# Optimization experiments

Measured on AMD Instinct MI355X. Metric: run time of the kernel, lower is better.

## Reference

```python
import jax, jax.numpy as jnp
import numpy as np

B, N = 4, 8192
EPS = 1e-5

def _gather(points, idx):
    # points: (B, N, C); idx: (B, ...) int -> (B, ..., C)
    return jax.vmap(lambda p, i: p[i])(points, idx)

def _square_distance(src, dst):
    # src: (B,S,3), dst: (B,N,3) -> (B,S,N)
    return (jnp.sum(src * src, -1)[..., None]
            + jnp.sum(dst * dst, -1)[:, None, :]
            - 2.0 * jnp.einsum('bsc,bnc->bsn', src, dst))

def _fps(xyz, npoint):
    # farthest point sampling, deterministic start at index 0
    b, n, _ = xyz.shape
    def step(carry, _):
        distance, farthest = carry
        centroid = _gather(xyz, farthest)                # (B,3)
        d = jnp.sum((xyz - centroid[:, None, :]) ** 2, -1)
        distance = jnp.minimum(distance, d)
        return (distance, jnp.argmax(distance, -1).astype(jnp.int32)), farthest
    init = (jnp.full((b, n), 1e10, xyz.dtype), jnp.zeros((b,), jnp.int32))
    _, idx = jax.lax.scan(step, init, None, length=npoint)
    return jnp.transpose(idx)                            # (B, npoint)

def _query_ball(radius, nsample, xyz, new_xyz):
    n = xyz.shape[1]
    sqrdists = _square_distance(new_xyz, xyz)            # (B,S,N)
    gi = jnp.where(sqrdists > radius * radius, n, jnp.arange(n, dtype=jnp.int32))
    gi = jnp.sort(gi, axis=-1)[:, :, :nsample]           # (B,S,K)
    first = gi[:, :, :1]
    return jnp.where(gi == n, first, gi)

def _set_abstraction(xyz, points, npoint, radius, nsample, w, bconv, gamma, beta):
    fps_idx = _fps(xyz, npoint)
    new_xyz = _gather(xyz, fps_idx)                      # (B,S,3)
    idx = _query_ball(radius, nsample, xyz, new_xyz)     # (B,S,K)
    grouped = _gather(xyz, idx) - new_xyz[:, :, None, :] # (B,S,K,3) centered
    if points is not None:
        grouped = jnp.concatenate([grouped, _gather(points, idx)], -1)
    # shared MLP = 1x1 Conv2d + BatchNorm2d (training batch stats) + ReLU
    h = jnp.einsum('bskc,cd->bskd', grouped, w) + bconv
    mu = jnp.mean(h, axis=(0, 1, 2))
    var = jnp.var(h, axis=(0, 1, 2))
    h = jax.nn.relu((h - mu) * jax.lax.rsqrt(var + EPS) * gamma + beta)
    return new_xyz, jnp.max(h, axis=2)                   # max-pool over nsample

def setup_inputs():
    key = jax.random.key(0)
    ks = jax.random.split(key, 5)
    return {
        'xyz': jax.random.uniform(ks[0], (B, N, 6), jnp.float32),
        'w1': jax.random.normal(ks[1], (6, 128), jnp.float32) * 0.1,
        'b1': jax.random.normal(ks[2], (128,), jnp.float32) * 0.01,
        'g1': jnp.ones((128,), jnp.float32),
        'be1': jnp.zeros((128,), jnp.float32),
        'w2': jax.random.normal(ks[3], (131, 693), jnp.float32) * 0.05,
        'b2': jax.random.normal(ks[4], (693,), jnp.float32) * 0.01,
        'g2': jnp.ones((693,), jnp.float32),
        'be2': jnp.zeros((693,), jnp.float32),
    }

def reference(xyz, w1, b1, g1, be1, w2, b2, g2, be2):
    coords, norm = xyz[:, :, :3], xyz[:, :, 3:]
    l1_xyz, l1_pts = _set_abstraction(coords, norm, 2048, 0.0025, 32, w1, b1, g1, be1)
    l2_xyz, l2_pts = _set_abstraction(l1_xyz, l1_pts, 256, 0.005, 16, w2, b2, g2, be2)
    return l2_xyz, l2_pts  # (B,256,3), (B,256,693)
```

## Files before the change

### kernel.cpp

```cpp
#include <hip/hip_runtime.h>
#include <hip/hip_bf16.h>

#define DEV __device__ __forceinline__

DEV float wave_max_f32(float v) {
#define STEPDPP(ctrl) { int iv = __float_as_int(v); \
    int sh = __builtin_amdgcn_update_dpp(iv, iv, ctrl, 0xf, 0xf, false); \
    v = fmaxf(v, __int_as_float(sh)); }
  STEPDPP(0x111)
  STEPDPP(0x112)
  STEPDPP(0x114)
  STEPDPP(0x118)
  STEPDPP(0x142)
  STEPDPP(0x143)
#undef STEPDPP
  return __int_as_float(__builtin_amdgcn_readlane(__float_as_int(v), 63));
}

__global__ void sentinel_k(float* out) {
  out[0] = 1000.0f;
}

__global__ __launch_bounds__(256) void zero_k(double* __restrict__ p, int n) {
  int i = blockIdx.x * 256 + threadIdx.x;
  if (i < n) p[i] = 0.0;
}

template<int PPT, int NPT, int NPTS, int STRIDE>
__global__ __launch_bounds__(512) void fps_k(const float* __restrict__ pts,
                                             float* __restrict__ out_xyz,
                                             float* __restrict__ out_f) {
  const int b = blockIdx.x, t = threadIdx.x;
  __shared__ unsigned long long wkey[2][8];
  __shared__ float wcx[2][8], wcy[2][8], wcz[2][8];
  float px[PPT], py[PPT], pz[PPT], dist[PPT];
  const int base = t * PPT;
  for (int j = 0; j < PPT; ++j) {
    const float* P = pts + (size_t)(b * NPTS + base + j) * STRIDE;
    px[j] = P[0]; py[j] = P[1]; pz[j] = P[2]; dist[j] = 1e10f;
  }
  if (t == 0) {
    wcx[1][0] = px[0]; wcy[1][0] = py[0]; wcz[1][0] = pz[0];
    size_t o = (size_t)b * NPT * 3;
    out_xyz[o] = px[0]; out_xyz[o+1] = py[0]; out_xyz[o+2] = pz[0];
    if (out_f) { out_f[o] = px[0]; out_f[o+1] = py[0]; out_f[o+2] = pz[0]; }
  }
  __syncthreads();
  float cx = wcx[1][0], cy = wcy[1][0], cz = wcz[1][0];
  const int lane = t & 63, wv = t >> 6;
  for (int s = 0; s < NPT - 1; ++s) {
    float vA = -1.0f, vB = -1.0f;
    int jA = 0, jB = PPT / 2;
    float axA = 0.f, ayA = 0.f, azA = 0.f, axB = 0.f, ayB = 0.f, azB = 0.f;
    {
#pragma clang fp contract(off)
      for (int j = 0; j < PPT / 2; ++j) {
        float dx = px[j] - cx, dy = py[j] - cy, dz = pz[j] - cz;
        float d = (dx*dx + dy*dy) + dz*dz;
        float dj = fminf(dist[j], d);
        dist[j] = dj;
        if (dj > vA) { vA = dj; jA = j; axA = px[j]; ayA = py[j]; azA = pz[j]; }
      }
      for (int j = PPT / 2; j < PPT; ++j) {
        float dx = px[j] - cx, dy = py[j] - cy, dz = pz[j] - cz;
        float d = (dx*dx + dy*dy) + dz*dz;
        float dj = fminf(dist[j], d);
        dist[j] = dj;
        if (dj > vB) { vB = dj; jB = j; axB = px[j]; ayB = py[j]; azB = pz[j]; }
      }
    }
    float vmax; int jb; float bx, by, bz;
    if (vB > vA) { vmax = vB; jb = jB; bx = axB; by = ayB; bz = azB; }
    else         { vmax = vA; jb = jA; bx = axA; by = ayA; bz = azA; }

    float wmax = wave_max_f32(vmax);
    unsigned long long mb = __ballot(vmax == wmax);
    int wl = __ffsll((unsigned long long)mb) - 1;
    const int p = s & 1;
    if (lane == wl) {
      wkey[p][wv] = ((unsigned long long)__float_as_uint(wmax) << 32) |
                    (unsigned long long)(0xFFFFFFFFu - (unsigned)(base + jb));
      wcx[p][wv] = bx; wcy[p][wv] = by; wcz[p][wv] = bz;
    }
    __syncthreads();
    unsigned long long bestk = wkey[p][0];
    int bw = 0;
#pragma unroll
    for (int w = 1; w < 8; ++w) {
      unsigned long long k2 = wkey[p][w];
      if (k2 > bestk) { bestk = k2; bw = w; }
    }
    cx = wcx[p][bw]; cy = wcy[p][bw]; cz = wcz[p][bw];
    if (t == 0) {
      size_t o = ((size_t)b * NPT + s + 1) * 3;
      out_xyz[o] = cx; out_xyz[o+1] = cy; out_xyz[o+2] = cz;
      if (out_f) { out_f[o] = cx; out_f[o+1] = cy; out_f[o+2] = cz; }
    }
  }
}

template<bool APPLY>
__global__ __launch_bounds__(256) void ball1_k(
    const float* __restrict__ xyz, const float* __restrict__ l1xyz,
    const float* __restrict__ w1, const float* __restrict__ b1,
    const double* __restrict__ A1, const double* __restrict__ B1,
    float* __restrict__ l1pts,
    double* __restrict__ S1R, double* __restrict__ S2R) {
  const int blk = blockIdx.x;
  const int b = blk >> 11, s = blk & 2047;
  const int t = threadIdx.x;
  __shared__ double w1s[768];
  __shared__ double b1s[128];
  __shared__ unsigned long long wm[4];
  __shared__ int lst[32];
  __shared__ double fls[32][6];
  __shared__ double red0[128], red1[128];

  for (int i = t; i < 768; i += 256) w1s[i] = (double)w1[i];
  if (t < 128) b1s[t] = (double)b1[t];

  const float* xb = xyz + (size_t)b * 8192 * 6;
  size_t co = ((size_t)b * 2048 + s) * 3;
  double cx = (double)l1xyz[co], cy = (double)l1xyz[co+1], cz = (double)l1xyz[co+2];

  const double R2 = 0.0025 * 0.0025;
  int cnt = 0;
  const int wvv = t >> 6, lane = t & 63;
  {
#pragma clang fp contract(off)
    double cs2 = (cx*cx + cy*cy) + cz*cz;
    for (int chunk = 0; chunk < 32 && cnt < 32; ++chunk) {
      int g = chunk * 256 + t;
      double x = (double)xb[(size_t)g*6];
      double y = (double)xb[(size_t)g*6+1];
      double z = (double)xb[(size_t)g*6+2];
      double pn2 = (x*x + y*y) + z*z;
      double dot = (cx*x + cy*y) + cz*z;
      double dsq = (cs2 + pn2) - 2.0 * dot;
      bool pred = !(dsq > R2);
      unsigned long long m = __ballot(pred);
      if (lane == 0) wm[wvv] = m;
      __syncthreads();
      int pre = 0, tot = 0;
      for (int w = 0; w < 4; ++w) {
        int c = __popcll(wm[w]);
        if (w < wvv) pre += c;
        tot += c;
      }
      if (pred) {
        int rank = cnt + pre + __popcll(m & ((1ull << lane) - 1ull));
        if (rank < 32) lst[rank] = g;
      }
      cnt += tot;
      __syncthreads();
    }
  }
  int cc = cnt < 32 ? cnt : 32;
  if (t >= cc && t < 32) lst[t] = lst[0];
  __syncthreads();
  if (t < 32) {
    int j = lst[t];
    fls[t][0] = (double)xb[(size_t)j*6]   - cx;
    fls[t][1] = (double)xb[(size_t)j*6+1] - cy;
    fls[t][2] = (double)xb[(size_t)j*6+2] - cz;
    fls[t][3] = (double)xb[(size_t)j*6+3];
    fls[t][4] = (double)xb[(size_t)j*6+4];
    fls[t][5] = (double)xb[(size_t)j*6+5];
  }
  __syncthreads();
  const int d = t & 127, kh = t >> 7;
  if (APPLY) {
    double a = A1[d], bb = B1[d];
    double vmax = -1e300;
    for (int k = kh; k < 32; k += 2) {
      double h = b1s[d];
#pragma unroll
      for (int c = 0; c < 6; ++c) h = fma(fls[k][c], w1s[c*128 + d], h);
      vmax = fmax(vmax, fma(a, h, bb));
    }
    if (kh == 1) red0[d] = vmax;
    __syncthreads();
    if (kh == 0) {
      double v = fmax(vmax, red0[d]);
      l1pts[((size_t)b * 2048 + s) * 128 + d] = (float)fmax(v, 0.0);
    }
  } else {
    double p1 = 0.0, p2 = 0.0;
    for (int k = kh; k < 32; k += 2) {
      double h = b1s[d];
#pragma unroll
      for (int c = 0; c < 6; ++c) h = fma(fls[k][c], w1s[c*128 + d], h);
      p1 += h; p2 = fma(h, h, p2);
    }
    if (kh == 1) { red0[d] = p1; red1[d] = p2; }
    __syncthreads();
    if (kh == 0) {
      int rep = blk & 7;
      atomicAdd(&S1R[(size_t)rep * 128 + d], p1 + red0[d]);
      atomicAdd(&S2R[(size_t)rep * 128 + d], p2 + red1[d]);
    }
  }
}

__global__ __launch_bounds__(256) void bn_finalize(const double* __restrict__ S1,
                                                   const double* __restrict__ S2,
                                                   int nrep, int D, double invN,
                                                   const float* __restrict__ g,
                                                   const float* __restrict__ be,
                                                   double* __restrict__ A, double* __restrict__ Bc) {
  int d = blockIdx.x * 256 + threadIdx.x;
  if (d >= D) return;
  double s1 = 0.0, s2 = 0.0;
  for (int r = 0; r < nrep; ++r) {
    s1 += S1[(size_t)r * D + d];
    s2 += S2[(size_t)r * D + d];
  }
  double mu = s1 * invN;
  double var = s2 * invN - mu * mu;
  double a = (double)g[d] / sqrt(var + 1e-5);
  A[d]  = a;
  Bc[d] = (double)be[d] - mu * a;
}

template<bool APPLY>
__global__ __launch_bounds__(256) void ball2_k(
    const float* __restrict__ l1xyz, const float* __restrict__ l1pts,
    const float* __restrict__ l2xyz,
    const float* __restrict__ w2, const float* __restrict__ b2,
    const double* __restrict__ A2, const double* __restrict__ B2,
    float* __restrict__ outp,
    double* __restrict__ T1R, double* __restrict__ T2R) {
  const int blk = blockIdx.x;
  const int b = blk >> 8, s = blk & 255;
  const int t = threadIdx.x;
  __shared__ double fT[131][16];
  __shared__ unsigned long long wm[4];
  __shared__ int lst[16];
  const float* Pb = l1xyz + (size_t)b * 2048 * 3;
  size_t co = ((size_t)b * 256 + s) * 3;
  double cx = (double)l2xyz[co], cy = (double)l2xyz[co+1], cz = (double)l2xyz[co+2];
  const double R2 = 0.005 * 0.005;
  int cnt = 0;
  const int wvv = t >> 6, lane = t & 63;
  {
#pragma clang fp contract(off)
    double cs2 = (cx*cx + cy*cy) + cz*cz;
    for (int chunk = 0; chunk < 8 && cnt < 16; ++chunk) {
      int g = chunk * 256 + t;
      double x = (double)Pb[(size_t)g*3];
      double y = (double)Pb[(size_t)g*3+1];
      double z = (double)Pb[(size_t)g*3+2];
      double pn2 = (x*x + y*y) + z*z;
      double dot = (cx*x + cy*y) + cz*z;
      double dsq = (cs2 + pn2) - 2.0 * dot;
      bool pred = !(dsq > R2);
      unsigned long long m = __ballot(pred);
      if (lane == 0) wm[wvv] = m;
      __syncthreads();
      int pre = 0, tot = 0;
      for (int w = 0; w < 4; ++w) {
        int c = __popcll(wm[w]);
        if (w < wvv) pre += c;
        tot += c;
      }
      if (pred) {
        int rank = cnt + pre + __popcll(m & ((1ull << lane) - 1ull));
        if (rank < 16) lst[rank] = g;
      }
      cnt += tot;
      __syncthreads();
    }
  }
  int cc = cnt < 16 ? cnt : 16;
  if (t >= cc && t < 16) lst[t] = lst[0];
  __syncthreads();
  for (int i = t; i < 16 * 131; i += 256) {
    int k = i & 15, c = i >> 4;
    int j = lst[k];
    double v;
    if (c == 0)      v = (double)Pb[(size_t)j*3]   - cx;
    else if (c == 1) v = (double)Pb[(size_t)j*3+1] - cy;
    else if (c == 2) v = (double)Pb[(size_t)j*3+2] - cz;
    else             v = (double)l1pts[((size_t)b*2048 + j)*128 + (c-3)];
    fT[c][k] = v;
  }
  __syncthreads();
  const int rep = blk & 7;
  for (int dd = 0; dd < 3; ++dd) {
    int d = t + dd * 256;
    if (d >= 693) break;
    double acc[16];
    double bv = (double)b2[d];
#pragma unroll
    for (int k = 0; k < 16; ++k) acc[k] = bv;
    for (int c = 0; c < 131; ++c) {
      double wv2 = (double)w2[(size_t)c * 693 + d];
#pragma unroll
      for (int k = 0; k < 16; ++k) acc[k] = fma(fT[c][k], wv2, acc[k]);
    }
    if (APPLY) {
      double a = A2[d], bb = B2[d];
      double vmax = -1e300;
#pragma unroll
      for (int k = 0; k < 16; ++k) vmax = fmax(vmax, fma(a, acc[k], bb));
      outp[((size_t)b * 256 + s) * 693 + d] = (float)fmax(vmax, 0.0);
    } else {
      double p1 = 0.0, p2 = 0.0;
#pragma unroll
      for (int k = 0; k < 16; ++k) { p1 += acc[k]; p2 = fma(acc[k], acc[k], p2); }
      atomicAdd(&T1R[(size_t)rep * 693 + d], p1);
      atomicAdd(&T2R[(size_t)rep * 693 + d], p2);
    }
  }
}

extern "C" void kernel_launch(void* const* d_in, const int* in_sizes, int n_in,
                              void* d_out, int out_size, void* d_ws, size_t ws_size,
                              hipStream_t stream) {
  (void)out_size;
  float* out = (float*)d_out;

  const int want[9] = {196608, 768, 128, 128, 128, 90783, 693, 693, 693};
  bool ok = (n_in == 9);
  for (int i = 0; ok && i < 9; ++i) ok = (in_sizes[i] == want[i]);
  const size_t REQ = 4600000;
  if (!ok || ws_size < REQ) {
    sentinel_k<<<1, 1, 0, stream>>>(out);
    return;
  }

  const float* xyz = (const float*)d_in[0];
  const float* w1  = (const float*)d_in[1];
  const float* b1  = (const float*)d_in[2];
  const float* g1  = (const float*)d_in[3];
  const float* be1 = (const float*)d_in[4];
  const float* w2  = (const float*)d_in[5];
  const float* b2  = (const float*)d_in[6];
  const float* g2  = (const float*)d_in[7];
  const float* be2 = (const float*)d_in[8];

  double* S1R = (double*)d_ws;
  double* S2R = S1R + 1024;
  double* T1R = S2R + 1024;
  double* T2R = T1R + 5544;
  double* A1  = T2R + 5544;
  double* B1  = A1 + 128;
  double* A2  = B1 + 128;
  double* B2  = A2 + 693;
  float* l1xyz = (float*)(B2 + 693);
  float* l2xyz = l1xyz + 24576;
  float* l1pts = l2xyz + 3072;

  zero_k<<<52, 256, 0, stream>>>(S1R, 13136);

  fps_k<16, 2048, 8192, 6><<<4, 512, 0, stream>>>(xyz, l1xyz, nullptr);
  fps_k<4, 256, 2048, 3><<<4, 512, 0, stream>>>(l1xyz, l2xyz, out);

  ball1_k<false><<<8192, 256, 0, stream>>>(xyz, l1xyz, w1, b1, nullptr, nullptr,
                                           nullptr, S1R, S2R);
  bn_finalize<<<1, 256, 0, stream>>>(S1R, S2R, 8, 128, 1.0 / (8192.0 * 32.0), g1, be1, A1, B1);
  ball1_k<true><<<8192, 256, 0, stream>>>(xyz, l1xyz, w1, b1, A1, B1,
                                          l1pts, S1R, S2R);

  ball2_k<false><<<1024, 256, 0, stream>>>(l1xyz, l1pts, l2xyz, w2, b2, nullptr, nullptr,
                                           nullptr, T1R, T2R);
  bn_finalize<<<3, 256, 0, stream>>>(T1R, T2R, 8, 693, 1.0 / (1024.0 * 16.0), g2, be2, A2, B2);
  ball2_k<true><<<1024, 256, 0, stream>>>(l1xyz, l1pts, l2xyz, w2, b2, A2, B2,
                                          out + 3072, T1R, T2R);
}
```

Measured before the change: 3.392 ms.

## Spatially bin points in FPS and skip distance updates for unreachable groups

Farthest point sampling now sorts each batch's points into an 8x8x8 grid with a shared-memory histogram and scan. Each thread then owns a spatially compact group and keeps that group's bounding sphere. A thread skips its distance-update loop when the new centroid is too far from its group to lower any of its current minimum distances. The block size drops from 512 to 256 threads, doubling points per thread, and the cross-wave reduction now uses 64-bit keys that break ties by point index. This cuts the serial per-step cost of FPS, at the price of setup work and divergence, and the gain depends on the spatial distribution of the input points.

```diff
diff --git a/kernel.cpp b/kernel.cpp
--- a/kernel.cpp
+++ b/kernel.cpp
@@ -2,20 +2,6 @@
 #include <hip/hip_bf16.h>
 
 #define DEV __device__ __forceinline__
-
-DEV float wave_max_f32(float v) {
-#define STEPDPP(ctrl) { int iv = __float_as_int(v); \
-    int sh = __builtin_amdgcn_update_dpp(iv, iv, ctrl, 0xf, 0xf, false); \
-    v = fmaxf(v, __int_as_float(sh)); }
-  STEPDPP(0x111)
-  STEPDPP(0x112)
-  STEPDPP(0x114)
-  STEPDPP(0x118)
-  STEPDPP(0x142)
-  STEPDPP(0x143)
-#undef STEPDPP
-  return __int_as_float(__builtin_amdgcn_readlane(__float_as_int(v), 63));
-}
 
 __global__ void sentinel_k(float* out) {
   out[0] = 1000.0f;
@@ -26,75 +12,164 @@
   if (i < n) p[i] = 0.0;
 }
 
-template<int PPT, int NPT, int NPTS, int STRIDE>
-__global__ __launch_bounds__(512) void fps_k(const float* __restrict__ pts,
-                                             float* __restrict__ out_xyz,
-                                             float* __restrict__ out_f) {
+template<int PPG, int NPT, int NPTS, int STRIDE>
+__global__ __launch_bounds__(256) void fps_quick_k(const float* __restrict__ pts,
+                                                   float* __restrict__ out_xyz,
+                                                   float* __restrict__ out_f) {
+  constexpr int T = 256;
+  constexpr int NW = T / 64;
+  static_assert(NPTS == T * PPG, "one group per thread");
   const int b = blockIdx.x, t = threadIdx.x;
-  __shared__ unsigned long long wkey[2][8];
-  __shared__ float wcx[2][8], wcy[2][8], wcz[2][8];
-  float px[PPT], py[PPT], pz[PPT], dist[PPT];
-  const int base = t * PPT;
-  for (int j = 0; j < PPT; ++j) {
-    const float* P = pts + (size_t)(b * NPTS + base + j) * STRIDE;
-    px[j] = P[0]; py[j] = P[1]; pz[j] = P[2]; dist[j] = 1e10f;
-  }
+  const int lane = t & 63, wv = t >> 6;
+
+  __shared__ int perm[NPTS];
+  __shared__ int hist[512];
+  __shared__ int base_[512];
+  __shared__ int wsum[NW];
+  __shared__ unsigned long long wkeyL[2][NW];
+  __shared__ float4 wc4[2][NW];
+
+  const float* Pb = pts + (size_t)b * NPTS * STRIDE;
+
+  for (int i = t; i < 512; i += T) hist[i] = 0;
+  __syncthreads();
+  int myCell[PPG];
+  for (int j = 0; j < PPG; ++j) {
+    int g = t * PPG + j;
+    float x = Pb[(size_t)g * STRIDE];
+    float y = Pb[(size_t)g * STRIDE + 1];
+    float z = Pb[(size_t)g * STRIDE + 2];
+    int ix = (int)(x * 8.0f); ix = ix < 0 ? 0 : (ix > 7 ? 7 : ix);
+    int iy = (int)(y * 8.0f); iy = iy < 0 ? 0 : (iy > 7 ? 7 : iy);
+    int iz = (int)(z * 8.0f); iz = iz < 0 ? 0 : (iz > 7 ? 7 : iz);
+    int cell = (ix << 6) | (iy << 3) | iz;
+    myCell[j] = cell;
+    atomicAdd(&hist[cell], 1);
+  }
+  __syncthreads();
+  {
+    int h0 = hist[2 * t], h1 = hist[2 * t + 1];
+    int s2 = h0 + h1;
+    int inc = s2;
+    for (int d = 1; d < 64; d <<= 1) {
+      int u = __shfl_up(inc, d);
+      if (lane >= d) inc += u;
+    }
+    if (lane == 63) wsum[wv] = inc;
+    __syncthreads();
+    int off = 0;
+#pragma unroll
+    for (int w = 0; w < NW; ++w) if (w < wv) off += wsum[w];
+    int excl = off + inc - s2;
+    base_[2 * t] = excl;
+    base_[2 * t + 1] = excl + h0;
+  }
+  __syncthreads();
+  for (int j = 0; j < PPG; ++j) {
+    int g = t * PPG + j;
+    int slot = atomicAdd(&base_[myCell[j]], 1);
+    perm[slot] = g;
+  }
+  __syncthreads();
+
+  float px[PPG], py[PPG], pz[PPG], dist[PPG];
+  float mnx = 1e30f, mny = 1e30f, mnz = 1e30f;
+  float mxx = -1e30f, mxy = -1e30f, mxz = -1e30f;
+  for (int j = 0; j < PPG; ++j) {
+    int g = perm[t * PPG + j];
+    float x = Pb[(size_t)g * STRIDE];
+    float y = Pb[(size_t)g * STRIDE + 1];
+    float z = Pb[(size_t)g * STRIDE + 2];
+    px[j] = x; py[j] = y; pz[j] = z; dist[j] = 1e10f;
+    mnx = fminf(mnx, x); mxx = fmaxf(mxx, x);
+    mny = fminf(mny, y); mxy = fmaxf(mxy, y);
+    mnz = fminf(mnz, z); mxz = fmaxf(mxz, z);
+  }
+  double bcx = 0.5 * ((double)mnx + (double)mxx);
+  double bcy = 0.5 * ((double)mny + (double)mxy);
+  double bcz = 0.5 * ((double)mnz + (double)mxz);
+  double r2m = 0.0;
+  for (int j = 0; j < PPG; ++j) {
+    double dx = (double)px[j] - bcx, dy = (double)py[j] - bcy, dz = (double)pz[j] - bcz;
+    double dd = fma(dx, dx, fma(dy, dy, dz * dz));
+    r2m = fmax(r2m, dd);
+  }
+  const double r = sqrt(r2m) * (1.0 + 1e-12) + 1e-300;
+
   if (t == 0) {
-    wcx[1][0] = px[0]; wcy[1][0] = py[0]; wcz[1][0] = pz[0];
+    float x0 = Pb[0], y0 = Pb[1], z0 = Pb[2];
+    wc4[1][0] = make_float4(x0, y0, z0, 0.0f);
     size_t o = (size_t)b * NPT * 3;
-    out_xyz[o] = px[0]; out_xyz[o+1] = py[0]; out_xyz[o+2] = pz[0];
-    if (out_f) { out_f[o] = px[0]; out_f[o+1] = py[0]; out_f[o+2] = pz[0]; }
-  }
-  __syncthreads();
-  float cx = wcx[1][0], cy = wcy[1][0], cz = wcz[1][0];
-  const int lane = t & 63, wv = t >> 6;
+    out_xyz[o] = x0; out_xyz[o + 1] = y0; out_xyz[o + 2] = z0;
+    if (out_f) { out_f[o] = x0; out_f[o + 1] = y0; out_f[o + 2] = z0; }
+  }
+  __syncthreads();
+  float ccx = wc4[1][0].x, ccy = wc4[1][0].y, ccz = wc4[1][0].z;
+
+  unsigned long long gkey = 0;
+  float gbx = 0.0f, gby = 0.0f, gbz = 0.0f;
+  double rs2 = 1e300;
+
   for (int s = 0; s < NPT - 1; ++s) {
-    float vA = -1.0f, vB = -1.0f;
-    int jA = 0, jB = PPT / 2;
-    float axA = 0.f, ayA = 0.f, azA = 0.f, axB = 0.f, ayB = 0.f, azB = 0.f;
-    {
+    const int p = s & 1;
+    double dxc = (double)ccx - bcx, dyc = (double)ccy - bcy, dzc = (double)ccz - bcz;
+    double tD = fma(dxc, dxc, fma(dyc, dyc, dzc * dzc));
+    if (tD < rs2) {
+      unsigned long long nk = 0;
+      float nbx = 0.0f, nby = 0.0f, nbz = 0.0f;
+      {
 #pragma clang fp contract(off)
-      for (int j = 0; j < PPT / 2; ++j) {
-        float dx = px[j] - cx, dy = py[j] - cy, dz = pz[j] - cz;
-        float d = (dx*dx + dy*dy) + dz*dz;
-        float dj = fminf(dist[j], d);
-        dist[j] = dj;
-        if (dj > vA) { vA = dj; jA = j; axA = px[j]; ayA = py[j]; azA = pz[j]; }
+        for (int j = 0; j < PPG; ++j) {
+          float dx = px[j] - ccx, dy = py[j] - ccy, dz = pz[j] - ccz;
+          float d = (dx * dx + dy * dy) + dz * dz;
+          float dj = fminf(dist[j], d);
+          dist[j] = dj;
+          int g = perm[t * PPG + j];
+          unsigned long long kj = ((unsigned long long)__float_as_uint(dj) << 32)
+                                | (unsigned long long)(0xFFFFFFFFu - (unsigned)g);
+          if (kj > nk) { nk = kj; nbx = px[j]; nby = py[j]; nbz = pz[j]; }
+        }
       }
-      for (int j = PPT / 2; j < PPT; ++j) {
-        float dx = px[j] - cx, dy = py[j] - cy, dz = pz[j] - cz;
-        float d = (dx*dx + dy*dy) + dz*dz;
-        float dj = fminf(dist[j], d);
-        dist[j] = dj;
-        if (dj > vB) { vB = dj; jB = j; axB = px[j]; ayB = py[j]; azB = pz[j]; }
-      }
-    }
-    float vmax; int jb; float bx, by, bz;
-    if (vB > vA) { vmax = vB; jb = jB; bx = axB; by = ayB; bz = azB; }
-    else         { vmax = vA; jb = jA; bx = axA; by = ayA; bz = azA; }
-
-    float wmax = wave_max_f32(vmax);
-    unsigned long long mb = __ballot(vmax == wmax);
-    int wl = __ffsll((unsigned long long)mb) - 1;
-    const int p = s & 1;
-    if (lane == wl) {
-      wkey[p][wv] = ((unsigned long long)__float_as_uint(wmax) << 32) |
-                    (unsigned long long)(0xFFFFFFFFu - (unsigned)(base + jb));
-      wcx[p][wv] = bx; wcy[p][wv] = by; wcz[p][wv] = bz;
+      gkey = nk; gbx = nbx; gby = nby; gbz = nbz;
+      float gmaxf = __uint_as_float((unsigned)(gkey >> 32));
+      double sg = sqrt((double)gmaxf * 1.000002 + 1e-300);
+      double rr = r + sg;
+      rs2 = rr * rr;
+    }
+
+    unsigned long long wk = gkey;
+#define STEP64(ctrl) { \
+    int lo_ = (int)(unsigned)wk, hi_ = (int)(unsigned)(wk >> 32); \
+    int slo_ = __builtin_amdgcn_update_dpp(lo_, lo_, ctrl, 0xf, 0xf, false); \
+    int shi_ = __builtin_amdgcn_update_dpp(hi_, hi_, ctrl, 0xf, 0xf, false); \
+    unsigned long long o_ = ((unsigned long long)(unsigned)shi_ << 32) | (unsigned)slo_; \
+    if (o_ > wk) wk = o_; }
+    STEP64(0x111)
+    STEP64(0x112)
+    STEP64(0x114)
+    STEP64(0x118)
+    STEP64(0x142)
+    STEP64(0x143)
+#undef STEP64
+    unsigned wlo = (unsigned)__builtin_amdgcn_readlane((int)(unsigned)wk, 63);
+    unsigned whi = (unsigned)__builtin_amdgcn_readlane((int)(unsigned)(wk >> 32), 63);
+    unsigned long long wmaxk = ((unsigned long long)whi << 32) | wlo;
+    if (gkey == wmaxk) {
+      wkeyL[p][wv] = gkey;
+      wc4[p][wv] = make_float4(gbx, gby, gbz, 0.0f);
     }
     __syncthreads();
-    unsigned long long bestk = wkey[p][0];
-    int bw = 0;
-#pragma unroll
-    for (int w = 1; w < 8; ++w) {
-      unsigned long long k2 = wkey[p][w];
-      if (k2 > bestk) { bestk = k2; bw = w; }
-    }
-    cx = wcx[p][bw]; cy = wcy[p][bw]; cz = wcz[p][bw];
+    unsigned long long k0 = wkeyL[p][0], k1 = wkeyL[p][1];
+    unsigned long long k2 = wkeyL[p][2], k3 = wkeyL[p][3];
+    float4 c0 = wc4[p][0], c1 = wc4[p][1], c2 = wc4[p][2], c3 = wc4[p][3];
+    if (k1 > k0) { k0 = k1; c0 = c1; }
+    if (k3 > k2) { k2 = k3; c2 = c3; }
+    if (k2 > k0) { k0 = k2; c0 = c2; }
+    ccx = c0.x; ccy = c0.y; ccz = c0.z;
     if (t == 0) {
       size_t o = ((size_t)b * NPT + s + 1) * 3;
-      out_xyz[o] = cx; out_xyz[o+1] = cy; out_xyz[o+2] = cz;
-      if (out_f) { out_f[o] = cx; out_f[o+1] = cy; out_f[o+2] = cz; }
+      out_xyz[o] = ccx; out_xyz[o + 1] = ccy; out_xyz[o + 2] = ccz;
+      if (out_f) { out_f[o] = ccx; out_f[o + 1] = ccy; out_f[o + 2] = ccz; }
     }
   }
 }
@@ -353,8 +428,8 @@
 
   zero_k<<<52, 256, 0, stream>>>(S1R, 13136);
 
-  fps_k<16, 2048, 8192, 6><<<4, 512, 0, stream>>>(xyz, l1xyz, nullptr);
-  fps_k<4, 256, 2048, 3><<<4, 512, 0, stream>>>(l1xyz, l2xyz, out);
+  fps_quick_k<32, 2048, 8192, 6><<<4, 256, 0, stream>>>(xyz, l1xyz, nullptr);
+  fps_quick_k<8, 256, 2048, 3><<<4, 256, 0, stream>>>(l1xyz, l2xyz, out);
 
   ball1_k<false><<<8192, 256, 0, stream>>>(xyz, l1xyz, w1, b1, nullptr, nullptr,
                                            nullptr, S1R, S2R);
```

After: 5.218 ms. +53.8%, slower.

## Streamline FPS per-step reduction and batch centroid output writes via LDS ring

Applied to the files above, without the earlier changes.

Reworks the farthest-point-sampling inner loop. The cross-wave reduction now packs value, index key and coordinates into one float4 plus a float and picks the winner with a tree of comparisons. A second wave-level max on the index runs only when several lanes tie. Centroid stores no longer go to global memory every step from thread 0; they go to a shared-memory ring and are flushed in batches of 64 by 192 threads, with loops fully unrolled. The goal is a shorter serial critical path per step, at the cost of more shared-memory traffic and extra flush logic.

```diff
diff --git a/kernel.cpp b/kernel.cpp
--- a/kernel.cpp
+++ b/kernel.cpp
@@ -17,6 +17,19 @@
   return __int_as_float(__builtin_amdgcn_readlane(__float_as_int(v), 63));
 }
 
+DEV unsigned wave_max_u32(unsigned v) {
+#define STEPDPPU(ctrl) { unsigned sh = (unsigned)__builtin_amdgcn_update_dpp((int)v, (int)v, ctrl, 0xf, 0xf, false); \
+    v = (sh > v) ? sh : v; }
+  STEPDPPU(0x111)
+  STEPDPPU(0x112)
+  STEPDPPU(0x114)
+  STEPDPPU(0x118)
+  STEPDPPU(0x142)
+  STEPDPPU(0x143)
+#undef STEPDPPU
+  return (unsigned)__builtin_amdgcn_readlane((int)v, 63);
+}
+
 __global__ void sentinel_k(float* out) {
   out[0] = 1000.0f;
 }
@@ -30,40 +43,50 @@
 __global__ __launch_bounds__(512) void fps_k(const float* __restrict__ pts,
                                              float* __restrict__ out_xyz,
                                              float* __restrict__ out_f) {
+  constexpr int NW = 8;
+  static_assert(NPTS == 512 * PPT, "one chunk per thread");
   const int b = blockIdx.x, t = threadIdx.x;
-  __shared__ unsigned long long wkey[2][8];
-  __shared__ float wcx[2][8], wcy[2][8], wcz[2][8];
+  const int lane = t & 63, wv = t >> 6;
+
+  __shared__ float4 wkc[2][NW];
+  __shared__ float wz[2][NW];
+  __shared__ float ring[128][3];
+
+  const float* Pb = pts + (size_t)b * NPTS * STRIDE;
   float px[PPT], py[PPT], pz[PPT], dist[PPT];
   const int base = t * PPT;
+#pragma unroll
   for (int j = 0; j < PPT; ++j) {
-    const float* P = pts + (size_t)(b * NPTS + base + j) * STRIDE;
+    const float* P = Pb + (size_t)(base + j) * STRIDE;
     px[j] = P[0]; py[j] = P[1]; pz[j] = P[2]; dist[j] = 1e10f;
   }
+
+  float ccx = Pb[0], ccy = Pb[1], ccz = Pb[2];
   if (t == 0) {
-    wcx[1][0] = px[0]; wcy[1][0] = py[0]; wcz[1][0] = pz[0];
     size_t o = (size_t)b * NPT * 3;
-    out_xyz[o] = px[0]; out_xyz[o+1] = py[0]; out_xyz[o+2] = pz[0];
-    if (out_f) { out_f[o] = px[0]; out_f[o+1] = py[0]; out_f[o+2] = pz[0]; }
-  }
-  __syncthreads();
-  float cx = wcx[1][0], cy = wcy[1][0], cz = wcz[1][0];
-  const int lane = t & 63, wv = t >> 6;
+    out_xyz[o] = ccx; out_xyz[o + 1] = ccy; out_xyz[o + 2] = ccz;
+    if (out_f) { out_f[o] = ccx; out_f[o + 1] = ccy; out_f[o + 2] = ccz; }
+  }
+
   for (int s = 0; s < NPT - 1; ++s) {
+    const int p = s & 1;
     float vA = -1.0f, vB = -1.0f;
     int jA = 0, jB = PPT / 2;
     float axA = 0.f, ayA = 0.f, azA = 0.f, axB = 0.f, ayB = 0.f, azB = 0.f;
     {
 #pragma clang fp contract(off)
+#pragma unroll
       for (int j = 0; j < PPT / 2; ++j) {
-        float dx = px[j] - cx, dy = py[j] - cy, dz = pz[j] - cz;
-        float d = (dx*dx + dy*dy) + dz*dz;
+        float dx = px[j] - ccx, dy = py[j] - ccy, dz = pz[j] - ccz;
+        float d = (dx * dx + dy * dy) + dz * dz;
         float dj = fminf(dist[j], d);
         dist[j] = dj;
         if (dj > vA) { vA = dj; jA = j; axA = px[j]; ayA = py[j]; azA = pz[j]; }
       }
+#pragma unroll
       for (int j = PPT / 2; j < PPT; ++j) {
-        float dx = px[j] - cx, dy = py[j] - cy, dz = pz[j] - cz;
-        float d = (dx*dx + dy*dy) + dz*dz;
+        float dx = px[j] - ccx, dy = py[j] - ccy, dz = pz[j] - ccz;
+        float d = (dx * dx + dy * dy) + dz * dz;
         float dj = fminf(dist[j], d);
         dist[j] = dj;
         if (dj > vB) { vB = dj; jB = j; axB = px[j]; ayB = py[j]; azB = pz[j]; }
@@ -72,29 +95,58 @@
     float vmax; int jb; float bx, by, bz;
     if (vB > vA) { vmax = vB; jb = jB; bx = axB; by = ayB; bz = azB; }
     else         { vmax = vA; jb = jA; bx = axA; by = ayA; bz = azA; }
-
-    float wmax = wave_max_f32(vmax);
-    unsigned long long mb = __ballot(vmax == wmax);
-    int wl = __ffsll((unsigned long long)mb) - 1;
-    const int p = s & 1;
-    if (lane == wl) {
-      wkey[p][wv] = ((unsigned long long)__float_as_uint(wmax) << 32) |
-                    (unsigned long long)(0xFFFFFFFFu - (unsigned)(base + jb));
-      wcx[p][wv] = bx; wcy[p][wv] = by; wcz[p][wv] = bz;
+    const unsigned klo = 0xFFFFFFFFu - (unsigned)(base + jb);
+
+    float wm = wave_max_f32(vmax);
+    unsigned long long mk = __ballot(vmax == wm);
+    bool iswin;
+    if (mk & (mk - 1)) {
+      unsigned lom = wave_max_u32((vmax == wm) ? klo : 0u);
+      iswin = (vmax == wm) && (klo == lom);
+    } else {
+      iswin = (vmax == wm);
+    }
+    if (iswin) {
+      wkc[p][wv] = make_float4(wm, __uint_as_float(klo), bx, by);
+      wz[p][wv] = bz;
     }
     __syncthreads();
-    unsigned long long bestk = wkey[p][0];
-    int bw = 0;
-#pragma unroll
-    for (int w = 1; w < 8; ++w) {
-      unsigned long long k2 = wkey[p][w];
-      if (k2 > bestk) { bestk = k2; bw = w; }
-    }
-    cx = wcx[p][bw]; cy = wcy[p][bw]; cz = wcz[p][bw];
+    if (s >= 64 && (s & 63) == 0 && t < 192) {
+      int j = s - 63 + t / 3, c = t % 3;
+      float v = ring[j & 127][c];
+      size_t o = ((size_t)b * NPT + j) * 3 + c;
+      out_xyz[o] = v;
+      if (out_f) out_f[o] = v;
+    }
+    float4 e0 = wkc[p][0], e1 = wkc[p][1], e2 = wkc[p][2], e3 = wkc[p][3];
+    float4 e4 = wkc[p][4], e5 = wkc[p][5], e6 = wkc[p][6], e7 = wkc[p][7];
+    float z0 = wz[p][0], z1 = wz[p][1], z2 = wz[p][2], z3 = wz[p][3];
+    float z4 = wz[p][4], z5 = wz[p][5], z6 = wz[p][6], z7 = wz[p][7];
+#define BETTER(A, B) (B.x > A.x || (B.x == A.x && __float_as_uint(B.y) > __float_as_uint(A.y)))
+    if (BETTER(e0, e1)) { e0 = e1; z0 = z1; }
+    if (BETTER(e2, e3)) { e2 = e3; z2 = z3; }
+    if (BETTER(e4, e5)) { e4 = e5; z4 = z5; }
+    if (BETTER(e6, e7)) { e6 = e7; z6 = z7; }
+    if (BETTER(e0, e2)) { e0 = e2; z0 = z2; }
+    if (BETTER(e4, e6)) { e4 = e6; z4 = z6; }
+    if (BETTER(e0, e4)) { e0 = e4; z0 = z4; }
+#undef BETTER
+    ccx = e0.z; ccy = e0.w; ccz = z0;
     if (t == 0) {
-      size_t o = ((size_t)b * NPT + s + 1) * 3;
-      out_xyz[o] = cx; out_xyz[o+1] = cy; out_xyz[o+2] = cz;
-      if (out_f) { out_f[o] = cx; out_f[o+1] = cy; out_f[o+2] = cz; }
+      int j = s + 1;
+      ring[j & 127][0] = ccx; ring[j & 127][1] = ccy; ring[j & 127][2] = ccz;
+    }
+  }
+  __syncthreads();
+  {
+    const int rstart = ((NPT - 2) & ~63) + 1;
+    const int nf = ((NPT - 1) - rstart + 1) * 3;
+    if (t < nf) {
+      int j = rstart + t / 3, c = t % 3;
+      float v = ring[j & 127][c];
+      size_t o = ((size_t)b * NPT + j) * 3 + c;
+      out_xyz[o] = v;
+      if (out_f) out_f[o] = v;
     }
   }
 }
```

New measurement: 4.032 ms. 1.19x slower.
